# Performance work log

Measured on AMD Instinct MI355X. Metric: run time of the kernel, lower is better.

## Reference

```python
import jax, jax.numpy as jnp
import numpy as np

B, T, C, H = 2, 2048, 1024, 16
D = C // H  # head dim = 64

def setup_inputs() -> dict:
    key = jax.random.key(0)
    ks = jax.random.split(key, 6)
    s = 0.02
    return {
        "x":  jax.random.normal(ks[0], (B, T, C), dtype=jnp.float32),
        "Wk": jax.random.normal(ks[1], (C, C), dtype=jnp.float32) * s,
        "Wq": jax.random.normal(ks[2], (C, C), dtype=jnp.float32) * s,
        "Wv": jax.random.normal(ks[3], (C, C), dtype=jnp.float32) * s,
        "Wp": jax.random.normal(ks[4], (C, C), dtype=jnp.float32) * s,
        "bp": jax.random.normal(ks[5], (C,), dtype=jnp.float32) * s,
    }

def reference(x, Wk, Wq, Wv, Wp, bp):
    Bs, Ts, Cs = x.shape
    # torch Linear: y = x @ W.T  (W is [out, in])
    def proj_heads(W):
        p = jnp.einsum('btc,dc->btd', x, W)
        return p.reshape(Bs, Ts, H, D).transpose(0, 2, 1, 3)  # [B,H,T,D]
    k = proj_heads(Wk)
    q = proj_heads(Wq)
    v = proj_heads(Wv)
    scale = 1.0 / jnp.sqrt(jnp.asarray(D, dtype=x.dtype))
    att = jnp.einsum('bhtd,bhsd->bhts', q, k) * scale  # [B,H,T,T]
    att = jax.nn.softmax(att, axis=-1)  # NOTE: no causal mask in the original forward
    y = jnp.einsum('bhts,bhsd->bhtd', att, v)
    y = y.transpose(0, 2, 1, 3).reshape(Bs, Ts, Cs)
    return jnp.einsum('btc,dc->btd', y, Wp) + bp
```

## Files before the change

kernel.cpp:

```cpp
#include <hip/hip_runtime.h>
#include <hip/hip_bf16.h>


typedef __bf16 bf16x8 __attribute__((ext_vector_type(8)));
typedef __bf16 bf16x4 __attribute__((ext_vector_type(4)));
typedef float  f32x4  __attribute__((ext_vector_type(4)));
typedef unsigned int uint2v __attribute__((ext_vector_type(2)));

#define QSCALE 0.18033688011112042f

__device__ __forceinline__ void gload_lds16(const void* g, void* l) {
  __builtin_amdgcn_global_load_lds((const __attribute__((address_space(1))) void*)g,
                                   (__attribute__((address_space(3))) void*)l, 16, 0, 0);
}
__device__ __forceinline__ unsigned int lds_off(const void* p) {
  return (unsigned int)(uintptr_t)(__attribute__((address_space(3))) const char*)p;
}
template<int IMM>
__device__ __forceinline__ uint2v tr_b64(unsigned int addr) {
  uint2v r;
  asm volatile("ds_read_b64_tr_b16 %0, %1 offset:%2" : "=v"(r) : "v"(addr), "i"(IMM));
  return r;
}

__global__ __launch_bounds__(256) void cvt_bf16(
    const float* __restrict__ x,  const float* __restrict__ wq, const float* __restrict__ wk,
    const float* __restrict__ wv, const float* __restrict__ wp,
    __bf16* __restrict__ xb,  __bf16* __restrict__ wqb, __bf16* __restrict__ wkb,
    __bf16* __restrict__ wvb, __bf16* __restrict__ wpb) {
  long long i = ((long long)blockIdx.x * 256 + threadIdx.x) * 4;
  const float* src; __bf16* dst; long long off;
  if      (i < 4194304LL) { src = x;  dst = xb;  off = i; }
  else if (i < 5242880LL) { src = wq; dst = wqb; off = i - 4194304LL; }
  else if (i < 6291456LL) { src = wk; dst = wkb; off = i - 5242880LL; }
  else if (i < 7340032LL) { src = wv; dst = wvb; off = i - 6291456LL; }
  else                    { src = wp; dst = wpb; off = i - 7340032LL; }
  float4 v = *(const float4*)(src + off);
  bf16x4 o;
  o[0] = (__bf16)v.x; o[1] = (__bf16)v.y; o[2] = (__bf16)v.z; o[3] = (__bf16)v.w;
  *(bf16x4*)(dst + off) = o;
}

template<int MFR>
__device__ __forceinline__ void gemm_core(
    const __bf16* __restrict__ A, const __bf16* __restrict__ Bw,
    int tileM, int tileN, char* smA, char* smB, f32x4 (&acc)[MFR][4]) {
  const int tid = threadIdx.x;
  const int lane = tid & 63;
  const int wid = tid >> 6;
  const int wr = wid >> 1, wc = wid & 1;
  #pragma unroll 1
  for (int k0 = 0; k0 < 1024; k0 += 64) {
    __syncthreads();
    #pragma unroll
    for (int r = 0; r < MFR; ++r) {
      int ci = tid + 256 * r;
      int row = ci >> 3, c = ci & 7;
      int sc = (c ^ (row & 7)) * 8;
      gload_lds16(A + (long long)(tileM + row) * 1024 + k0 + sc, smA + ci * 16);
    }
    #pragma unroll
    for (int r = 0; r < 4; ++r) {
      int ci = tid + 256 * r;
      int row = ci >> 3, c = ci & 7;
      int sc = (c ^ (row & 7)) * 8;
      gload_lds16(Bw + (long long)(tileN + row) * 1024 + k0 + sc, smB + ci * 16);
    }
    __syncthreads();
    #pragma unroll
    for (int kk = 0; kk < 2; ++kk) {
      bf16x8 af[MFR], bfr[4];
      #pragma unroll
      for (int i = 0; i < MFR; ++i) {
        int mrow = wr * (MFR * 16) + i * 16 + (lane & 15);
        af[i] = *(const bf16x8*)(smA + mrow * 128 +
                  ((kk * 64 + (lane >> 4) * 16) ^ ((mrow & 7) << 4)));
      }
      #pragma unroll
      for (int i = 0; i < 4; ++i) {
        int nrow = wc * 64 + i * 16 + (lane & 15);
        bfr[i] = *(const bf16x8*)(smB + nrow * 128 +
                  ((kk * 64 + (lane >> 4) * 16) ^ ((nrow & 7) << 4)));
      }
      __builtin_amdgcn_s_setprio(1);
      #pragma unroll
      for (int mi = 0; mi < MFR; ++mi)
        #pragma unroll
        for (int ni = 0; ni < 4; ++ni)
          acc[mi][ni] = __builtin_amdgcn_mfma_f32_16x16x32_bf16(af[mi], bfr[ni], acc[mi][ni], 0, 0, 0);
      __builtin_amdgcn_s_setprio(0);
    }
  }
}

__global__ __launch_bounds__(256) void gemm_qkv(
    const __bf16* __restrict__ Xb, const __bf16* __restrict__ Wqb,
    const __bf16* __restrict__ Wkb, const __bf16* __restrict__ Wvb,
    __bf16* __restrict__ Qh, __bf16* __restrict__ Kh, __bf16* __restrict__ Vh) {
  __shared__ __align__(16) char smA[16384];
  __shared__ __align__(16) char smB[16384];
  const int z = blockIdx.z;
  const __bf16* W = (z == 0) ? Wqb : (z == 1) ? Wkb : Wvb;
  __bf16* dst     = (z == 0) ? Qh  : (z == 1) ? Kh  : Vh;
  const float scale = (z == 0) ? QSCALE : 1.0f;
  const int tileM = blockIdx.x * 128, tileN = blockIdx.y * 128;
  f32x4 acc[4][4] = {};
  gemm_core<4>(Xb, W, tileM, tileN, smA, smB, acc);
  const int lane = threadIdx.x & 63, wid = threadIdx.x >> 6;
  const int wr = wid >> 1, wc = wid & 1;
  #pragma unroll
  for (int mi = 0; mi < 4; ++mi) {
    #pragma unroll
    for (int ni = 0; ni < 4; ++ni) {
      int n = tileN + wc * 64 + ni * 16 + (lane & 15);
      int h = n >> 6, d = n & 63;
      #pragma unroll
      for (int r = 0; r < 4; ++r) {
        int m = tileM + wr * 64 + mi * 16 + (lane >> 4) * 4 + r;
        int b = m >> 11, t = m & 2047;
        dst[((b * 16 + h) * 2048 + t) * 64 + d] = (__bf16)(acc[mi][ni][r] * scale);
      }
    }
  }
}

__global__ __launch_bounds__(256) void gemm_proj(
    const __bf16* __restrict__ Yb, const __bf16* __restrict__ Wpb,
    const float* __restrict__ bias, float* __restrict__ out) {
  __shared__ __align__(16) char smA[8192];
  __shared__ __align__(16) char smB[16384];
  const int tileM = blockIdx.x * 64, tileN = blockIdx.y * 128;
  f32x4 acc[2][4] = {};
  gemm_core<2>(Yb, Wpb, tileM, tileN, smA, smB, acc);
  const int lane = threadIdx.x & 63, wid = threadIdx.x >> 6;
  const int wr = wid >> 1, wc = wid & 1;
  #pragma unroll
  for (int mi = 0; mi < 2; ++mi) {
    #pragma unroll
    for (int ni = 0; ni < 4; ++ni) {
      int n = tileN + wc * 64 + ni * 16 + (lane & 15);
      float bv = bias[n];
      #pragma unroll
      for (int r = 0; r < 4; ++r) {
        int m = tileM + wr * 32 + mi * 16 + (lane >> 4) * 4 + r;
        out[(long long)m * 1024 + n] = acc[mi][ni][r] + bv;
      }
    }
  }
}

template<int KS>
__device__ __forceinline__ void pv_half(unsigned int trP, unsigned int trV,
                                        f32x4 Oa[2][4], f32x4 Osum[2], bf16x8 ones) {
  uint2v pl[2], ph[2];
  pl[0] = tr_b64<0 * 2048 + KS * 1024      >(trP);
  ph[0] = tr_b64<0 * 2048 + KS * 1024 + 512>(trP);
  pl[1] = tr_b64<1 * 2048 + KS * 1024      >(trP);
  ph[1] = tr_b64<1 * 2048 + KS * 1024 + 512>(trP);
  uint2v t0[4], t1[4];
  t0[0] = tr_b64<KS * 1024 + 0 * 2048>(trV);  t1[0] = tr_b64<KS * 1024 + 0 * 2048 + 512>(trV);
  t0[1] = tr_b64<KS * 1024 + 1 * 2048>(trV);  t1[1] = tr_b64<KS * 1024 + 1 * 2048 + 512>(trV);
  t0[2] = tr_b64<KS * 1024 + 2 * 2048>(trV);  t1[2] = tr_b64<KS * 1024 + 2 * 2048 + 512>(trV);
  t0[3] = tr_b64<KS * 1024 + 3 * 2048>(trV);  t1[3] = tr_b64<KS * 1024 + 3 * 2048 + 512>(trV);
  asm volatile("s_waitcnt lgkmcnt(0)");
  __builtin_amdgcn_sched_barrier(0);
  __builtin_amdgcn_s_setprio(1);
  bf16x8 pa[2];
  #pragma unroll
  for (int mi = 0; mi < 2; ++mi) {
    uint4 u; u.x = pl[mi][0]; u.y = pl[mi][1]; u.z = ph[mi][0]; u.w = ph[mi][1];
    pa[mi] = __builtin_bit_cast(bf16x8, u);
    Osum[mi] = __builtin_amdgcn_mfma_f32_16x16x32_bf16(pa[mi], ones, Osum[mi], 0, 0, 0);
  }
  #pragma unroll
  for (int nd = 0; nd < 4; ++nd) {
    uint4 u; u.x = t0[nd][0]; u.y = t0[nd][1]; u.z = t1[nd][0]; u.w = t1[nd][1];
    bf16x8 vf = __builtin_bit_cast(bf16x8, u);
    #pragma unroll
    for (int mi = 0; mi < 2; ++mi)
      Oa[mi][nd] = __builtin_amdgcn_mfma_f32_16x16x32_bf16(pa[mi], vf, Oa[mi][nd], 0, 0, 0);
  }
  __builtin_amdgcn_s_setprio(0);
}

__global__ __launch_bounds__(512, 4) void attn(
    const __bf16* __restrict__ Qh, const __bf16* __restrict__ Kh,
    const __bf16* __restrict__ Vh, float* __restrict__ Opart,
    float* __restrict__ lpart) {
  __shared__ __align__(16) char Ksm[2][8192];
  __shared__ __align__(16) char Vsm[2][8192];
  __shared__ __align__(16) char Psm[32768];
  const int tid = threadIdx.x, lane = tid & 63, wid = tid >> 6;
  const int lo = lane & 15, hi = lane >> 4;
  const int bh = blockIdx.x;
  const int qb = blockIdx.y;
  const int split = blockIdx.z;
  const int base = bh * (2048 * 64);
  const int qrow0 = qb * 256 + wid * 32;
  const int key0 = split * 1024;

  bf16x8 qf[2][2];
  #pragma unroll
  for (int mi = 0; mi < 2; ++mi)
    #pragma unroll
    for (int kk = 0; kk < 2; ++kk)
      qf[mi][kk] = *(const bf16x8*)(Qh + base + (qrow0 + mi * 16 + lo) * 64
                                    + kk * 32 + hi * 8);

  bf16x8 ones;
  #pragma unroll
  for (int j = 0; j < 8; ++j) ones[j] = (__bf16)1.0f;

  f32x4 Oa[2][4] = {};
  f32x4 Osum[2] = {};
  const unsigned int trP = lds_off(Psm) + wid * 4096 + lane * 8;

  unsigned int koff[4];
  #pragma unroll
  for (int ni = 0; ni < 4; ++ni) {
    int row = ni * 16 + lo;
    koff[ni] = row * 128 + ((hi * 16) ^ ((row & 7) << 4));
  }
  unsigned int paddr[2][4];
  #pragma unroll
  for (int mi = 0; mi < 2; ++mi)
    #pragma unroll
    for (int ni = 0; ni < 4; ++ni) {
      int kq = ni * 16 + lo;
      paddr[mi][ni] = wid * 4096 + mi * 2048 + (kq >> 5) * 1024 + ((kq >> 2) & 1) * 512 +
                      ((kq >> 3) & 3) * 128 + (kq & 3) * 32 + hi * 8;
    }

  int krow = tid >> 3, kc = tid & 7;
  int ksrc = base + (key0 + krow) * 64 + (kc ^ (krow & 7)) * 8;
  int kdst = tid * 16;
  int vcc = tid >> 6, vks = vcc & 1, vd4 = vcc >> 1;
  int vkey = vks * 32 + ((lane >> 3) & 3) * 8 + ((lane >> 5) & 1) * 4 + ((lane >> 1) & 3);
  int vsrc = base + (key0 + vkey) * 64 + vd4 * 16 + (lane & 1) * 8;
  int vdst = vks * 1024 + vd4 * 2048 + lane * 16;

  gload_lds16(Kh + ksrc, &Ksm[0][0] + kdst);
  gload_lds16(Vh + vsrc, &Vsm[0][0] + vdst);
  __syncthreads();
  int buf = 0;

  #pragma unroll 1
  for (int kt = 0; kt < 16; ++kt) {
    if (kt < 15) {
      gload_lds16(Kh + ksrc + (kt + 1) * 4096, &Ksm[buf ^ 1][0] + kdst);
      gload_lds16(Vh + vsrc + (kt + 1) * 4096, &Vsm[buf ^ 1][0] + vdst);
    }
    __builtin_amdgcn_sched_barrier(0);

    const char* Kb = &Ksm[buf][0];
    const unsigned int trV = lds_off(Vsm) + buf * 8192 + lane * 8;

    f32x4 S[2][4] = {};
    #pragma unroll
    for (int kk = 0; kk < 2; ++kk) {
      bf16x8 kf[4];
      #pragma unroll
      for (int ni = 0; ni < 4; ++ni)
        kf[ni] = *(const bf16x8*)(Kb + (koff[ni] ^ (kk * 64)));
      __builtin_amdgcn_s_setprio(1);
      #pragma unroll
      for (int mi = 0; mi < 2; ++mi)
        #pragma unroll
        for (int ni = 0; ni < 4; ++ni)
          S[mi][ni] = __builtin_amdgcn_mfma_f32_16x16x32_bf16(qf[mi][kk], kf[ni], S[mi][ni], 0, 0, 0);
      __builtin_amdgcn_s_setprio(0);
    }

    #pragma unroll
    for (int mi = 0; mi < 2; ++mi) {
      #pragma unroll
      for (int ni = 0; ni < 4; ++ni) {
        bf16x4 pb;
        #pragma unroll
        for (int r = 0; r < 4; ++r) pb[r] = (__bf16)exp2f(S[mi][ni][r]);
        *(bf16x4*)(&Psm[0] + paddr[mi][ni]) = pb;
      }
    }

    pv_half<0>(trP, trV, Oa, Osum, ones);
    pv_half<1>(trP, trV, Oa, Osum, ones);

    __syncthreads();
    buf ^= 1;
  }

  float* Op = Opart + (long long)(split * 32 + bh) * 2048 * 64;
  float* lp = lpart + (split * 32 + bh) * 2048;
  #pragma unroll
  for (int mi = 0; mi < 2; ++mi) {
    #pragma unroll
    for (int r = 0; r < 4; ++r) {
      int t = qrow0 + mi * 16 + hi * 4 + r;
      if (lo == 0) lp[t] = Osum[mi][r];
      #pragma unroll
      for (int nd = 0; nd < 4; ++nd)
        Op[(long long)t * 64 + nd * 16 + lo] = Oa[mi][nd][r];
    }
  }
}

__global__ __launch_bounds__(256) void attn_combine(
    const float* __restrict__ Opart, const float* __restrict__ lpart,
    __bf16* __restrict__ Yb) {
  int i = blockIdx.x * 256 + threadIdx.x;
  int row = i >> 4;
  int d0 = (i & 15) * 4;
  float4 o0 = *(const float4*)(Opart + (long long)row * 64 + d0);
  float4 o1 = *(const float4*)(Opart + 4194304LL + (long long)row * 64 + d0);
  float inv = 1.0f / (lpart[row] + lpart[65536 + row]);
  int bh = row >> 11, t = row & 2047;
  int b = bh >> 4, h = bh & 15;
  bf16x4 o;
  o[0] = (__bf16)((o0.x + o1.x) * inv); o[1] = (__bf16)((o0.y + o1.y) * inv);
  o[2] = (__bf16)((o0.z + o1.z) * inv); o[3] = (__bf16)((o0.w + o1.w) * inv);
  *(bf16x4*)(Yb + ((long long)(b * 2048 + t)) * 1024 + h * 64 + d0) = o;
}

extern "C" void kernel_launch(void* const* d_in, const int* in_sizes, int n_in,
                              void* d_out, int out_size, void* d_ws, size_t ws_size,
                              hipStream_t stream) {
  const float* x  = (const float*)d_in[0];
  const float* Wk = (const float*)d_in[1];
  const float* Wq = (const float*)d_in[2];
  const float* Wv = (const float*)d_in[3];
  const float* Wp = (const float*)d_in[4];
  const float* bp = (const float*)d_in[5];
  float* out = (float*)d_out;

  char* ws = (char*)d_ws;
  __bf16* Xb  = (__bf16*)ws;
  __bf16* Wqb = Xb  + 4194304;
  __bf16* Wkb = Wqb + 1048576;
  __bf16* Wvb = Wkb + 1048576;
  __bf16* Wpb = Wvb + 1048576;
  __bf16* Qh  = Wpb + 1048576;
  __bf16* Kh  = Qh  + 4194304;
  __bf16* Vh  = Kh  + 4194304;
  __bf16* Yb  = Vh  + 4194304;
  float*  Opart = (float*)(Yb + 4194304);
  float*  lpart = Opart + 8388608;

  cvt_bf16<<<8192, 256, 0, stream>>>(x, Wq, Wk, Wv, Wp, Xb, Wqb, Wkb, Wvb, Wpb);
  gemm_qkv<<<dim3(32, 8, 3), 256, 0, stream>>>(Xb, Wqb, Wkb, Wvb, Qh, Kh, Vh);
  attn<<<dim3(32, 8, 2), 512, 0, stream>>>(Qh, Kh, Vh, Opart, lpart);
  attn_combine<<<4096, 256, 0, stream>>>(Opart, lpart, Yb);
  gemm_proj<<<dim3(64, 8), 256, 0, stream>>>(Yb, Wpb, bp, out);
}
```

Measured before the change: 189.2 us.

## Drop split-K attention and combine kernel; each warp owns 16 query rows over all keys

The attention kernel no longer splits keys across two blocks. Each block now covers 128 query rows with 16 rows per warp, loops over all 32 key tiles, and normalizes and writes bf16 output directly, so the fp32 partial buffers and the combine kernel are gone. This removes a launch and the partial-result global traffic, and halves the P buffer in LDS. The exp results are also packed with v_cvt_pk_bf16_f32, and the occupancy hint rises to 6 blocks. In exchange each warp does half the QK and PV MFMA work per K/V tile load, so K/V reuse from LDS is lower and the serial key loop is twice as long.

```diff
diff --git a/kernel.cpp b/kernel.cpp
--- a/kernel.cpp
+++ b/kernel.cpp
@@ -20,6 +20,11 @@
 __device__ __forceinline__ uint2v tr_b64(unsigned int addr) {
   uint2v r;
   asm volatile("ds_read_b64_tr_b16 %0, %1 offset:%2" : "=v"(r) : "v"(addr), "i"(IMM));
+  return r;
+}
+__device__ __forceinline__ unsigned int cvtpk_bf16(float a, float b) {
+  unsigned int r;
+  asm("v_cvt_pk_bf16_f32 %0, %1, %2" : "=v"(r) : "v"(a), "v"(b));
   return r;
 }
 
@@ -42,7 +47,7 @@
 }
 
 template<int MFR>
-__device__ __forceinline__ void gemm_core(
+__device__ __forceinline__ void gemm_core_sb(
     const __bf16* __restrict__ A, const __bf16* __restrict__ Bw,
     int tileM, int tileN, char* smA, char* smB, f32x4 (&acc)[MFR][4]) {
   const int tid = threadIdx.x;
@@ -105,7 +110,7 @@
   const float scale = (z == 0) ? QSCALE : 1.0f;
   const int tileM = blockIdx.x * 128, tileN = blockIdx.y * 128;
   f32x4 acc[4][4] = {};
-  gemm_core<4>(Xb, W, tileM, tileN, smA, smB, acc);
+  gemm_core_sb<4>(Xb, W, tileM, tileN, smA, smB, acc);
   const int lane = threadIdx.x & 63, wid = threadIdx.x >> 6;
   const int wr = wid >> 1, wc = wid & 1;
   #pragma unroll
@@ -131,7 +136,7 @@
   __shared__ __align__(16) char smB[16384];
   const int tileM = blockIdx.x * 64, tileN = blockIdx.y * 128;
   f32x4 acc[2][4] = {};
-  gemm_core<2>(Yb, Wpb, tileM, tileN, smA, smB, acc);
+  gemm_core_sb<2>(Yb, Wpb, tileM, tileN, smA, smB, acc);
   const int lane = threadIdx.x & 63, wid = threadIdx.x >> 6;
   const int wr = wid >> 1, wc = wid & 1;
   #pragma unroll
@@ -151,12 +156,10 @@
 
 template<int KS>
 __device__ __forceinline__ void pv_half(unsigned int trP, unsigned int trV,
-                                        f32x4 Oa[2][4], f32x4 Osum[2], bf16x8 ones) {
-  uint2v pl[2], ph[2];
-  pl[0] = tr_b64<0 * 2048 + KS * 1024      >(trP);
-  ph[0] = tr_b64<0 * 2048 + KS * 1024 + 512>(trP);
-  pl[1] = tr_b64<1 * 2048 + KS * 1024      >(trP);
-  ph[1] = tr_b64<1 * 2048 + KS * 1024 + 512>(trP);
+                                        f32x4 (&Oa)[4], f32x4& Osum, bf16x8 ones) {
+  uint2v pl, ph;
+  pl = tr_b64<KS * 1024      >(trP);
+  ph = tr_b64<KS * 1024 + 512>(trP);
   uint2v t0[4], t1[4];
   t0[0] = tr_b64<KS * 1024 + 0 * 2048>(trV);  t1[0] = tr_b64<KS * 1024 + 0 * 2048 + 512>(trV);
   t0[1] = tr_b64<KS * 1024 + 1 * 2048>(trV);  t1[1] = tr_b64<KS * 1024 + 1 * 2048 + 512>(trV);
@@ -165,55 +168,43 @@
   asm volatile("s_waitcnt lgkmcnt(0)");
   __builtin_amdgcn_sched_barrier(0);
   __builtin_amdgcn_s_setprio(1);
-  bf16x8 pa[2];
-  #pragma unroll
-  for (int mi = 0; mi < 2; ++mi) {
-    uint4 u; u.x = pl[mi][0]; u.y = pl[mi][1]; u.z = ph[mi][0]; u.w = ph[mi][1];
-    pa[mi] = __builtin_bit_cast(bf16x8, u);
-    Osum[mi] = __builtin_amdgcn_mfma_f32_16x16x32_bf16(pa[mi], ones, Osum[mi], 0, 0, 0);
-  }
+  uint4 up; up.x = pl[0]; up.y = pl[1]; up.z = ph[0]; up.w = ph[1];
+  bf16x8 pa = __builtin_bit_cast(bf16x8, up);
+  Osum = __builtin_amdgcn_mfma_f32_16x16x32_bf16(pa, ones, Osum, 0, 0, 0);
   #pragma unroll
   for (int nd = 0; nd < 4; ++nd) {
     uint4 u; u.x = t0[nd][0]; u.y = t0[nd][1]; u.z = t1[nd][0]; u.w = t1[nd][1];
     bf16x8 vf = __builtin_bit_cast(bf16x8, u);
-    #pragma unroll
-    for (int mi = 0; mi < 2; ++mi)
-      Oa[mi][nd] = __builtin_amdgcn_mfma_f32_16x16x32_bf16(pa[mi], vf, Oa[mi][nd], 0, 0, 0);
+    Oa[nd] = __builtin_amdgcn_mfma_f32_16x16x32_bf16(pa, vf, Oa[nd], 0, 0, 0);
   }
   __builtin_amdgcn_s_setprio(0);
 }
 
-__global__ __launch_bounds__(512, 4) void attn(
+__global__ __launch_bounds__(512, 6) void attn(
     const __bf16* __restrict__ Qh, const __bf16* __restrict__ Kh,
-    const __bf16* __restrict__ Vh, float* __restrict__ Opart,
-    float* __restrict__ lpart) {
+    const __bf16* __restrict__ Vh, __bf16* __restrict__ Yb) {
   __shared__ __align__(16) char Ksm[2][8192];
   __shared__ __align__(16) char Vsm[2][8192];
-  __shared__ __align__(16) char Psm[32768];
+  __shared__ __align__(16) char Psm[16384];
   const int tid = threadIdx.x, lane = tid & 63, wid = tid >> 6;
   const int lo = lane & 15, hi = lane >> 4;
   const int bh = blockIdx.x;
   const int qb = blockIdx.y;
-  const int split = blockIdx.z;
   const int base = bh * (2048 * 64);
-  const int qrow0 = qb * 256 + wid * 32;
-  const int key0 = split * 1024;
-
-  bf16x8 qf[2][2];
-  #pragma unroll
-  for (int mi = 0; mi < 2; ++mi)
-    #pragma unroll
-    for (int kk = 0; kk < 2; ++kk)
-      qf[mi][kk] = *(const bf16x8*)(Qh + base + (qrow0 + mi * 16 + lo) * 64
-                                    + kk * 32 + hi * 8);
+  const int qrow0 = qb * 128 + wid * 16;
+
+  bf16x8 qf[2];
+  #pragma unroll
+  for (int kk = 0; kk < 2; ++kk)
+    qf[kk] = *(const bf16x8*)(Qh + base + (qrow0 + lo) * 64 + kk * 32 + hi * 8);
 
   bf16x8 ones;
   #pragma unroll
   for (int j = 0; j < 8; ++j) ones[j] = (__bf16)1.0f;
 
-  f32x4 Oa[2][4] = {};
-  f32x4 Osum[2] = {};
-  const unsigned int trP = lds_off(Psm) + wid * 4096 + lane * 8;
+  f32x4 Oa[4] = {};
+  f32x4 Osum = {};
+  const unsigned int trP = lds_off(Psm) + wid * 2048 + lane * 8;
 
   unsigned int koff[4];
   #pragma unroll
@@ -221,22 +212,20 @@
     int row = ni * 16 + lo;
     koff[ni] = row * 128 + ((hi * 16) ^ ((row & 7) << 4));
   }
-  unsigned int paddr[2][4];
-  #pragma unroll
-  for (int mi = 0; mi < 2; ++mi)
-    #pragma unroll
-    for (int ni = 0; ni < 4; ++ni) {
-      int kq = ni * 16 + lo;
-      paddr[mi][ni] = wid * 4096 + mi * 2048 + (kq >> 5) * 1024 + ((kq >> 2) & 1) * 512 +
-                      ((kq >> 3) & 3) * 128 + (kq & 3) * 32 + hi * 8;
-    }
+  unsigned int paddr[4];
+  #pragma unroll
+  for (int ni = 0; ni < 4; ++ni) {
+    int kq = ni * 16 + lo;
+    paddr[ni] = wid * 2048 + (kq >> 5) * 1024 + ((kq >> 2) & 1) * 512 +
+                ((kq >> 3) & 3) * 128 + (kq & 3) * 32 + hi * 8;
+  }
 
   int krow = tid >> 3, kc = tid & 7;
-  int ksrc = base + (key0 + krow) * 64 + (kc ^ (krow & 7)) * 8;
+  int ksrc = base + krow * 64 + (kc ^ (krow & 7)) * 8;
   int kdst = tid * 16;
   int vcc = tid >> 6, vks = vcc & 1, vd4 = vcc >> 1;
   int vkey = vks * 32 + ((lane >> 3) & 3) * 8 + ((lane >> 5) & 1) * 4 + ((lane >> 1) & 3);
-  int vsrc = base + (key0 + vkey) * 64 + vd4 * 16 + (lane & 1) * 8;
+  int vsrc = base + vkey * 64 + vd4 * 16 + (lane & 1) * 8;
   int vdst = vks * 1024 + vd4 * 2048 + lane * 16;
 
   gload_lds16(Kh + ksrc, &Ksm[0][0] + kdst);
@@ -245,8 +234,8 @@
   int buf = 0;
 
   #pragma unroll 1
-  for (int kt = 0; kt < 16; ++kt) {
-    if (kt < 15) {
+  for (int kt = 0; kt < 32; ++kt) {
+    if (kt < 31) {
       gload_lds16(Kh + ksrc + (kt + 1) * 4096, &Ksm[buf ^ 1][0] + kdst);
       gload_lds16(Vh + vsrc + (kt + 1) * 4096, &Vsm[buf ^ 1][0] + vdst);
     }
@@ -255,7 +244,7 @@
     const char* Kb = &Ksm[buf][0];
     const unsigned int trV = lds_off(Vsm) + buf * 8192 + lane * 8;
 
-    f32x4 S[2][4] = {};
+    f32x4 S[4] = {};
     #pragma unroll
     for (int kk = 0; kk < 2; ++kk) {
       bf16x8 kf[4];
@@ -264,22 +253,21 @@
         kf[ni] = *(const bf16x8*)(Kb + (koff[ni] ^ (kk * 64)));
       __builtin_amdgcn_s_setprio(1);
       #pragma unroll
-      for (int mi = 0; mi < 2; ++mi)
-        #pragma unroll
-        for (int ni = 0; ni < 4; ++ni)
-          S[mi][ni] = __builtin_amdgcn_mfma_f32_16x16x32_bf16(qf[mi][kk], kf[ni], S[mi][ni], 0, 0, 0);
+      for (int ni = 0; ni < 4; ++ni)
+        S[ni] = __builtin_amdgcn_mfma_f32_16x16x32_bf16(qf[kk], kf[ni], S[ni], 0, 0, 0);
       __builtin_amdgcn_s_setprio(0);
     }
 
     #pragma unroll
-    for (int mi = 0; mi < 2; ++mi) {
-      #pragma unroll
-      for (int ni = 0; ni < 4; ++ni) {
-        bf16x4 pb;
-        #pragma unroll
-        for (int r = 0; r < 4; ++r) pb[r] = (__bf16)exp2f(S[mi][ni][r]);
-        *(bf16x4*)(&Psm[0] + paddr[mi][ni]) = pb;
-      }
+    for (int ni = 0; ni < 4; ++ni) {
+      float e0 = exp2f(S[ni][0]);
+      float e1 = exp2f(S[ni][1]);
+      float e2 = exp2f(S[ni][2]);
+      float e3 = exp2f(S[ni][3]);
+      uint2v w;
+      w[0] = cvtpk_bf16(e0, e1);
+      w[1] = cvtpk_bf16(e2, e3);
+      *(uint2v*)(&Psm[0] + paddr[ni]) = w;
     }
 
     pv_half<0>(trP, trV, Oa, Osum, ones);
@@ -289,36 +277,15 @@
     buf ^= 1;
   }
 
-  float* Op = Opart + (long long)(split * 32 + bh) * 2048 * 64;
-  float* lp = lpart + (split * 32 + bh) * 2048;
-  #pragma unroll
-  for (int mi = 0; mi < 2; ++mi) {
-    #pragma unroll
-    for (int r = 0; r < 4; ++r) {
-      int t = qrow0 + mi * 16 + hi * 4 + r;
-      if (lo == 0) lp[t] = Osum[mi][r];
-      #pragma unroll
-      for (int nd = 0; nd < 4; ++nd)
-        Op[(long long)t * 64 + nd * 16 + lo] = Oa[mi][nd][r];
-    }
-  }
-}
-
-__global__ __launch_bounds__(256) void attn_combine(
-    const float* __restrict__ Opart, const float* __restrict__ lpart,
-    __bf16* __restrict__ Yb) {
-  int i = blockIdx.x * 256 + threadIdx.x;
-  int row = i >> 4;
-  int d0 = (i & 15) * 4;
-  float4 o0 = *(const float4*)(Opart + (long long)row * 64 + d0);
-  float4 o1 = *(const float4*)(Opart + 4194304LL + (long long)row * 64 + d0);
-  float inv = 1.0f / (lpart[row] + lpart[65536 + row]);
-  int bh = row >> 11, t = row & 2047;
-  int b = bh >> 4, h = bh & 15;
-  bf16x4 o;
-  o[0] = (__bf16)((o0.x + o1.x) * inv); o[1] = (__bf16)((o0.y + o1.y) * inv);
-  o[2] = (__bf16)((o0.z + o1.z) * inv); o[3] = (__bf16)((o0.w + o1.w) * inv);
-  *(bf16x4*)(Yb + ((long long)(b * 2048 + t)) * 1024 + h * 64 + d0) = o;
+  const int b = bh >> 4, h = bh & 15;
+  #pragma unroll
+  for (int r = 0; r < 4; ++r) {
+    float inv = 1.0f / Osum[r];
+    int t = qrow0 + hi * 4 + r;
+    #pragma unroll
+    for (int nd = 0; nd < 4; ++nd)
+      Yb[(b * 2048 + t) * 1024 + h * 64 + nd * 16 + lo] = (__bf16)(Oa[nd][r] * inv);
+  }
 }
 
 extern "C" void kernel_launch(void* const* d_in, const int* in_sizes, int n_in,
@@ -342,12 +309,9 @@
   __bf16* Kh  = Qh  + 4194304;
   __bf16* Vh  = Kh  + 4194304;
   __bf16* Yb  = Vh  + 4194304;
-  float*  Opart = (float*)(Yb + 4194304);
-  float*  lpart = Opart + 8388608;
 
   cvt_bf16<<<8192, 256, 0, stream>>>(x, Wq, Wk, Wv, Wp, Xb, Wqb, Wkb, Wvb, Wpb);
   gemm_qkv<<<dim3(32, 8, 3), 256, 0, stream>>>(Xb, Wqb, Wkb, Wvb, Qh, Kh, Vh);
-  attn<<<dim3(32, 8, 2), 512, 0, stream>>>(Qh, Kh, Vh, Opart, lpart);
-  attn_combine<<<4096, 256, 0, stream>>>(Opart, lpart, Yb);
+  attn<<<dim3(32, 16), 512, 0, stream>>>(Qh, Kh, Vh, Yb);
   gemm_proj<<<dim3(64, 8), 256, 0, stream>>>(Yb, Wpb, bp, out);
 }
```

Measured after the change: 190.0 us. About the same (+0.4%).
